# Kernel optimization log

Hardware: AMD Instinct MI355X
Metric: run time of the kernel (lower is better)

The kernel has to match this reference:

```python
import jax, jax.numpy as jnp
import numpy as np
from jax import lax

DIM = 128
N_CODEBOOKS = 8
CODEBOOK_SIZE = 2048
BATCH = 16
TOKENS = 2048


def setup_inputs() -> dict:
    key = jax.random.key(0)
    k1, k2 = jax.random.split(key)
    x = jax.random.normal(k1, (BATCH, DIM, TOKENS), dtype=jnp.float32)
    # matches nn.Parameter(torch.randn(K, D) / D**0.5) per stage, stacked
    codebooks = jax.random.normal(k2, (N_CODEBOOKS, CODEBOOK_SIZE, DIM),
                                  dtype=jnp.float32) / jnp.sqrt(jnp.float32(DIM))
    return {"x": x, "codebooks": codebooks}


def reference(x, codebooks):
    """Residual VQ forward.

    x: (B, D, T), codebooks: (n_cb, K, D)
    Returns (total_quantized (B,D,T), codes (B,n_cb,T) int32, commitment_loss scalar)
    """
    xt = jnp.transpose(x, (0, 2, 1))  # (B, T, D)

    def step(carry, cb):
        residual, total = carry  # (B,T,D) each; cb: (K,D)
        # squared euclidean distances: ||r||^2 - 2 r.c + ||c||^2 -> (B,T,K)
        dist = (jnp.sum(residual * residual, axis=-1, keepdims=True)
                - 2.0 * jnp.einsum('btd,kd->btk', residual, cb)
                + jnp.sum(cb * cb, axis=-1))
        idx = jnp.argmin(dist, axis=-1)          # (B, T)
        quantized = cb[idx]                       # gather -> (B, T, D)
        # straight-through combine
        q_st = residual + lax.stop_gradient(quantized - residual)
        total = total + q_st
        residual = residual - lax.stop_gradient(quantized)
        # F.mse_loss(residual.detach(), zeros) == mean(residual**2), detached
        loss = jnp.mean(lax.stop_gradient(residual) ** 2)
        return (residual, total), (idx.astype(jnp.int32), loss)

    init = (xt, jnp.zeros_like(xt))
    (_, total), (codes, losses) = lax.scan(step, init, codebooks)
    total_quantized = jnp.transpose(total, (0, 2, 1))   # (B, D, T)
    codes = jnp.transpose(codes, (1, 0, 2))             # (B, n_cb, T)
    commitment_loss = jnp.sum(losses)
    return total_quantized, codes, commitment_loss
```

## Files before the change

kernel.cpp:

```cpp
#include <hip/hip_runtime.h>

#define DIM 128
#define NCB 8
#define KSZ 2048
#define BATCH 16
#define TOK 2048
#define NTOK (BATCH * TOK)
#define NELEM (BATCH * DIM * TOK)
#define T_TILE 128
#define NTHR 512
#define CHUNK 32
#define NCHUNK 16
#define GCODES 512

typedef float f32x4 __attribute__((ext_vector_type(4)));
typedef _Float16 f16x8 __attribute__((ext_vector_type(8)));

__global__ void rvq_prep_f16(const float* __restrict__ cbs,
                             _Float16* __restrict__ chf) {
    int i = blockIdx.x * 256 + threadIdx.x;
    chf[i] = (_Float16)cbs[i];
}

__global__ void rvq_cnorm(const float* __restrict__ cbs,
                          float* __restrict__ cnorm,
                          float* __restrict__ loss_acc) {
    if (blockIdx.x == 0 && threadIdx.x == 0) *loss_acc = 0.0f;
    int k = blockIdx.x * 256 + threadIdx.x;
    const float4* row = (const float4*)(cbs + (size_t)k * DIM);
    float s = 0.0f;
#pragma unroll
    for (int i = 0; i < DIM / 4; ++i) {
        float4 v = row[i];
        s += v.x * v.x + v.y * v.y + v.z * v.z + v.w * v.w;
    }
    cnorm[k] = s;
}

__global__ __launch_bounds__(NTHR, 2) void rvq_fused(
        const float* __restrict__ x,
        const float* __restrict__ cbs,
        const _Float16* __restrict__ chf,
        const float* __restrict__ cng,
        float* __restrict__ out,
        float* __restrict__ codes,
        float* __restrict__ loss_acc) {
    __shared__ float res_lds[T_TILE][DIM + 4];
    __shared__ __align__(16) char shbuf[T_TILE * 144 * 4];
    __shared__ float cn_lds[KSZ];

    _Float16* Ball = (_Float16*)shbuf;
    float*    cand = (float*)shbuf;

    const int tid   = threadIdx.x;
    const int lane  = tid & 63;
    const int wv    = __builtin_amdgcn_readfirstlane(tid >> 6);
    const int col16 = lane & 15;
    const int quad  = lane >> 4;
    const int g     = wv >> 1;
    const int sub   = wv & 1;

    const int token0 = blockIdx.x * T_TILE;
    const int b      = token0 >> 11;
    const int t_in_b = token0 & (TOK - 1);

    {
        const float* xb = x + (size_t)b * DIM * TOK + t_in_b;
#pragma unroll
        for (int it = 0; it < 8; ++it) {
            int idx = it * NTHR + tid;
            int d  = idx >> 5;
            int t4 = (idx & 31) * 4;
            float4 v = *(const float4*)(xb + (size_t)d * TOK + t4);
            res_lds[t4 + 0][d] = v.x;
            res_lds[t4 + 1][d] = v.y;
            res_lds[t4 + 2][d] = v.z;
            res_lds[t4 + 3][d] = v.w;
        }
    }
    __syncthreads();

    float my_loss = 0.0f;
    const float INFV = __builtin_inff();

#pragma unroll 1
    for (int s = 0; s < NCB; ++s) {
        const _Float16* __restrict__ ch_s = chf + (size_t)s * KSZ * DIM;
        const float* __restrict__ cb_s = cbs + (size_t)s * KSZ * DIM;
        const float* __restrict__ cn_s = cng + (size_t)s * KSZ;

        {
            float4 v = *(const float4*)(cn_s + tid * 4);
            *(float4*)&cn_lds[tid * 4] = v;
        }

        f16x8 ah[4][4];
#pragma unroll
        for (int mt = 0; mt < 4; ++mt) {
#pragma unroll
            for (int dc = 0; dc < 4; ++dc) {
                int t  = sub * 64 + mt * 16 + col16;
                int d0 = dc * 32 + quad * 8;
                float4 u = *(const float4*)&res_lds[t][d0];
                float4 w = *(const float4*)&res_lds[t][d0 + 4];
                f16x8 hv;
                hv[0] = (_Float16)u.x; hv[1] = (_Float16)u.y;
                hv[2] = (_Float16)u.z; hv[3] = (_Float16)u.w;
                hv[4] = (_Float16)w.x; hv[5] = (_Float16)w.y;
                hv[6] = (_Float16)w.z; hv[7] = (_Float16)w.w;
                ah[mt][dc] = hv;
            }
        }

        float k1[16], k2[16];
#pragma unroll
        for (int sl = 0; sl < 16; ++sl) { k1[sl] = INFV; k2[sl] = INFV; }

        f16x8 stg[4];
        _Float16* Bg = Ball + g * 2 * 4096;

#pragma unroll
        for (int j = 0; j < 4; ++j) {
            int f = sub * 4 + j;
            int nt = f >> 2, dc = f & 3;
            stg[j] = *(const f16x8*)(ch_s +
                (size_t)(g * GCODES + nt * 16 + col16) * DIM + dc * 32 + quad * 8);
        }
#pragma unroll
        for (int j = 0; j < 4; ++j) {
            int f = sub * 4 + j;
            *(f16x8*)(Bg + f * 512 + lane * 8) = stg[j];
        }
        __syncthreads();

        f32x4 acc[4][2];
#pragma unroll 1
        for (int c = 0; c < NCHUNK; ++c) {
            const int cur = c & 1;
            if (c < NCHUNK - 1) {
#pragma unroll
                for (int j = 0; j < 4; ++j) {
                    int f = sub * 4 + j;
                    int nt = f >> 2, dc = f & 3;
                    stg[j] = *(const f16x8*)(ch_s +
                        (size_t)(g * GCODES + (c + 1) * CHUNK + nt * 16 + col16) * DIM
                        + dc * 32 + quad * 8);
                }
            }
#pragma unroll
            for (int mt = 0; mt < 4; ++mt) {
                acc[mt][0] = (f32x4){0.f, 0.f, 0.f, 0.f};
                acc[mt][1] = (f32x4){0.f, 0.f, 0.f, 0.f};
            }
#pragma unroll
            for (int dc = 0; dc < 4; ++dc) {
                f16x8 b0 = *(const f16x8*)(Bg + cur * 4096 + dc * 512 + lane * 8);
                f16x8 b1 = *(const f16x8*)(Bg + cur * 4096 + (4 + dc) * 512 + lane * 8);
#pragma unroll
                for (int mt = 0; mt < 4; ++mt) {
                    acc[mt][0] = __builtin_amdgcn_mfma_f32_16x16x32_f16(
                        ah[mt][dc], b0, acc[mt][0], 0, 0, 0);
                    acc[mt][1] = __builtin_amdgcn_mfma_f32_16x16x32_f16(
                        ah[mt][dc], b1, acc[mt][1], 0, 0, 0);
                }
            }
            {
                float cn0 = cn_lds[g * GCODES + c * CHUNK + col16];
                float cn1 = cn_lds[g * GCODES + c * CHUNK + 16 + col16];
                unsigned em = (unsigned)(c << 1);
#pragma unroll
                for (int mt = 0; mt < 4; ++mt) {
#pragma unroll
                    for (int r = 0; r < 4; ++r) {
                        float p0 = fmaf(-2.0f, acc[mt][0][r], cn0);
                        float p1 = fmaf(-2.0f, acc[mt][1][r], cn1);
                        float q0 = __uint_as_float(
                            (__float_as_uint(p0) & 0xFFFFFFE0u) | em);
                        float q1 = __uint_as_float(
                            (__float_as_uint(p1) & 0xFFFFFFE0u) | em | 1u);
                        float m = fminf(q0, q1);
                        int sl = mt * 4 + r;
                        k2[sl] = fminf(k2[sl], fmaxf(k1[sl], m));
                        k1[sl] = fminf(k1[sl], m);
                    }
                }
            }
            if (c < NCHUNK - 1) {
#pragma unroll
                for (int j = 0; j < 4; ++j) {
                    int f = sub * 4 + j;
                    *(f16x8*)(Bg + (cur ^ 1) * 4096 + f * 512 + lane * 8) = stg[j];
                }
            }
            __syncthreads();
        }

#pragma unroll
        for (int mt = 0; mt < 4; ++mt) {
#pragma unroll
            for (int r = 0; r < 4; ++r) {
                int t = sub * 64 + mt * 16 + quad * 4 + r;
                int sl = mt * 4 + r;
                float2 pr; pr.x = k1[sl]; pr.y = k2[sl];
                *(float2*)&cand[t * 144 + g * 36 + col16 * 2] = pr;
            }
        }
        __syncthreads();

        {
            const int t  = tid >> 2;
            const int gg = tid & 3;
            float bk[4];
            int   bcol[4];
#pragma unroll
            for (int jj = 0; jj < 4; ++jj) { bk[jj] = INFV; bcol[jj] = 0; }
            const float* base = &cand[t * 144 + gg * 36];
#pragma unroll
            for (int j = 0; j < 8; ++j) {
                float4 v4 = *(const float4*)(base + j * 4);
                float vv[4] = {v4.x, v4.y, v4.z, v4.w};
#pragma unroll
                for (int e = 0; e < 4; ++e) {
                    float v = vv[e];
                    int col = (j * 4 + e) >> 1;
#pragma unroll
                    for (int jj = 0; jj < 4; ++jj) {
                        bool lt = v < bk[jj];
                        float tv = bk[jj]; int tc = bcol[jj];
                        bk[jj] = lt ? v : bk[jj];
                        bcol[jj] = lt ? col : bcol[jj];
                        v = lt ? tv : v;
                        col = lt ? tc : col;
                    }
                }
            }
            int cds[4];
#pragma unroll
            for (int jj = 0; jj < 4; ++jj) {
                unsigned e = __float_as_uint(bk[jj]) & 0x1Fu;
                cds[jj] = gg * GCODES + (int)((e >> 1) << 5) +
                          (int)((e & 1) << 4) + bcol[jj];
            }
            const float* p0 = cb_s + (size_t)cds[0] * DIM;
            const float* p1 = cb_s + (size_t)cds[1] * DIM;
            const float* p2 = cb_s + (size_t)cds[2] * DIM;
            const float* p3 = cb_s + (size_t)cds[3] * DIM;
            float n0 = 0, n1 = 0, n2 = 0, n3 = 0;
            float a[4][4];
#pragma unroll
            for (int jj = 0; jj < 4; ++jj)
#pragma unroll
                for (int e = 0; e < 4; ++e) a[jj][e] = 0.0f;
#pragma unroll 8
            for (int d4 = 0; d4 < DIM / 4; ++d4) {
                float4 r4 = *(const float4*)&res_lds[t][d4 * 4];
                n0 = fmaf(r4.x, r4.x, n0); n1 = fmaf(r4.y, r4.y, n1);
                n2 = fmaf(r4.z, r4.z, n2); n3 = fmaf(r4.w, r4.w, n3);
                float4 q0 = *(const float4*)(p0 + d4 * 4);
                a[0][0] = fmaf(r4.x, q0.x, a[0][0]);
                a[0][1] = fmaf(r4.y, q0.y, a[0][1]);
                a[0][2] = fmaf(r4.z, q0.z, a[0][2]);
                a[0][3] = fmaf(r4.w, q0.w, a[0][3]);
                float4 q1 = *(const float4*)(p1 + d4 * 4);
                a[1][0] = fmaf(r4.x, q1.x, a[1][0]);
                a[1][1] = fmaf(r4.y, q1.y, a[1][1]);
                a[1][2] = fmaf(r4.z, q1.z, a[1][2]);
                a[1][3] = fmaf(r4.w, q1.w, a[1][3]);
                float4 q2 = *(const float4*)(p2 + d4 * 4);
                a[2][0] = fmaf(r4.x, q2.x, a[2][0]);
                a[2][1] = fmaf(r4.y, q2.y, a[2][1]);
                a[2][2] = fmaf(r4.z, q2.z, a[2][2]);
                a[2][3] = fmaf(r4.w, q2.w, a[2][3]);
                float4 q3 = *(const float4*)(p3 + d4 * 4);
                a[3][0] = fmaf(r4.x, q3.x, a[3][0]);
                a[3][1] = fmaf(r4.y, q3.y, a[3][1]);
                a[3][2] = fmaf(r4.z, q3.z, a[3][2]);
                a[3][3] = fmaf(r4.w, q3.w, a[3][3]);
            }
            float rn = (n0 + n1) + (n2 + n3);
            float bd = INFV; int bc = 0x7FFFFFFF;
#pragma unroll
            for (int jj = 0; jj < 4; ++jj) {
                float dot = (a[jj][0] + a[jj][1]) + (a[jj][2] + a[jj][3]);
                float dist = fmaf(-2.0f, dot, rn) + cn_s[cds[jj]];
                if (dist < bd || (dist == bd && cds[jj] < bc)) {
                    bd = dist; bc = cds[jj];
                }
            }
#pragma unroll
            for (int mk = 1; mk <= 2; mk <<= 1) {
                float od = __shfl_xor(bd, mk, 64);
                int   oc = __shfl_xor(bc, mk, 64);
                if (od < bd || (od == bd && oc < bc)) { bd = od; bc = oc; }
            }
            if (gg == 0)
                codes[(size_t)b * (NCB * TOK) + (size_t)s * TOK + t_in_b + t] =
                    (float)bc;
            const float* qrow = cb_s + (size_t)bc * DIM;
            float lp = 0.0f;
#pragma unroll
            for (int d4 = 0; d4 < 8; ++d4) {
                int d = gg * 32 + d4 * 4;
                float4 r4 = *(const float4*)&res_lds[t][d];
                float4 q4 = *(const float4*)(qrow + d);
                float4 nr;
                nr.x = r4.x - q4.x; nr.y = r4.y - q4.y;
                nr.z = r4.z - q4.z; nr.w = r4.w - q4.w;
                *(float4*)&res_lds[t][d] = nr;
                lp += nr.x * nr.x + nr.y * nr.y + nr.z * nr.z + nr.w * nr.w;
            }
            my_loss += lp;
        }
        __syncthreads();
    }

    {
        const float* xb = x + (size_t)b * DIM * TOK + t_in_b;
        float* ob = out + (size_t)b * DIM * TOK + t_in_b;
#pragma unroll
        for (int it = 0; it < 8; ++it) {
            int idx = it * NTHR + tid;
            int d  = idx >> 5;
            int t4 = (idx & 31) * 4;
            float4 v = *(const float4*)(xb + (size_t)d * TOK + t4);
            float4 o;
            o.x = v.x - res_lds[t4 + 0][d];
            o.y = v.y - res_lds[t4 + 1][d];
            o.z = v.z - res_lds[t4 + 2][d];
            o.w = v.w - res_lds[t4 + 3][d];
            *(float4*)(ob + (size_t)d * TOK + t4) = o;
        }
    }

#pragma unroll
    for (int off = 32; off > 0; off >>= 1)
        my_loss += __shfl_down(my_loss, off, 64);
    if (lane == 0) atomicAdd(loss_acc, my_loss);
}

__global__ void rvq_loss_fin(const float* __restrict__ loss_acc,
                             float* __restrict__ loss_out) {
    *loss_out = *loss_acc * (1.0f / (float)NELEM);
}

extern "C" void kernel_launch(void* const* d_in, const int* in_sizes, int n_in,
                              void* d_out, int out_size, void* d_ws, size_t ws_size,
                              hipStream_t stream) {
    const float* x   = (const float*)d_in[0];
    const float* cbs = (const float*)d_in[1];

    float* out      = (float*)d_out;
    float* codes    = out + NELEM;
    float* loss_out = out + NELEM + (size_t)BATCH * NCB * TOK;

    float* wsf      = (float*)d_ws;
    float* loss_acc = wsf;
    _Float16* chf   = (_Float16*)(wsf + 256);
    float* cng      = (float*)(chf + (size_t)NCB * KSZ * DIM);

    hipLaunchKernelGGL(rvq_prep_f16, dim3((NCB * KSZ * DIM) / 256), dim3(256),
                       0, stream, cbs, chf);
    hipLaunchKernelGGL(rvq_cnorm, dim3((NCB * KSZ) / 256), dim3(256), 0, stream,
                       cbs, cng, loss_acc);
    hipLaunchKernelGGL(rvq_fused, dim3(NTOK / T_TILE), dim3(NTHR), 0, stream,
                       x, cbs, chf, cng, out, codes, loss_acc);
    hipLaunchKernelGGL(rvq_loss_fin, dim3(1), dim3(1), 0, stream,
                       loss_acc, loss_out);
}
```

Baseline: 603.6 us.

## Load codebook fragments directly from global into registers, drop LDS staging

The f16 codebook fragments now go straight from global memory into MFMA B-operand registers with double-buffered register sets (bA/bB), replacing the LDS staging buffer and the per-chunk __syncthreads. The full 9-bit code index is packed into the low mantissa bits of each distance, so the top-2 tracking and final top-4 selection no longer carry separate column indices and use min/max networks. This removes LDS traffic and barriers from the inner loop, and the candidate buffer shrinks. The cost is more global/L2 loads, because the two waves in each pair now each load the full fragment set, plus higher register pressure and coarser distance precision from truncating 9 mantissa bits.

Measured after the change: 606.3 us. About the same (+0.4%).

```diff
diff --git a/kernel.cpp b/kernel.cpp
--- a/kernel.cpp
+++ b/kernel.cpp
@@ -46,11 +46,8 @@
         float* __restrict__ codes,
         float* __restrict__ loss_acc) {
     __shared__ float res_lds[T_TILE][DIM + 4];
-    __shared__ __align__(16) char shbuf[T_TILE * 144 * 4];
+    __shared__ float cand[T_TILE * 132];
     __shared__ float cn_lds[KSZ];
-
-    _Float16* Ball = (_Float16*)shbuf;
-    float*    cand = (float*)shbuf;
 
     const int tid   = threadIdx.x;
     const int lane  = tid & 63;
@@ -83,16 +80,71 @@
     float my_loss = 0.0f;
     const float INFV = __builtin_inff();
 
+#define LOADB(dst)                                                             \
+    {                                                                          \
+        _Pragma("unroll")                                                      \
+        for (int dc = 0; dc < 4; ++dc) {                                       \
+            dst[dc]     = *(const f16x8*)(p0 + dc * 32);                       \
+            dst[4 + dc] = *(const f16x8*)(p1 + dc * 32);                       \
+        }                                                                      \
+    }
+
+#define COMPUTE(bX)                                                            \
+    {                                                                          \
+        _Pragma("unroll")                                                      \
+        for (int mt = 0; mt < 4; ++mt) {                                       \
+            acc[mt][0] = (f32x4){0.f, 0.f, 0.f, 0.f};                          \
+            acc[mt][1] = (f32x4){0.f, 0.f, 0.f, 0.f};                          \
+        }                                                                      \
+        _Pragma("unroll")                                                      \
+        for (int dc = 0; dc < 4; ++dc) {                                       \
+            _Pragma("unroll")                                                  \
+            for (int mt = 0; mt < 4; ++mt) {                                   \
+                acc[mt][0] = __builtin_amdgcn_mfma_f32_16x16x32_f16(           \
+                    ah[mt][dc], bX[dc], acc[mt][0], 0, 0, 0);                  \
+                acc[mt][1] = __builtin_amdgcn_mfma_f32_16x16x32_f16(           \
+                    ah[mt][dc], bX[4 + dc], acc[mt][1], 0, 0, 0);              \
+            }                                                                  \
+        }                                                                      \
+    }
+
+#define FOLD(cc)                                                               \
+    {                                                                          \
+        float cn0 = cn_lds[g * GCODES + (cc) * CHUNK + col16];                 \
+        float cn1 = cn_lds[g * GCODES + (cc) * CHUNK + 16 + col16];            \
+        unsigned em0 = ((unsigned)(cc) << 5) | (unsigned)col16;                \
+        unsigned em1 = em0 | 16u;                                              \
+        _Pragma("unroll")                                                      \
+        for (int mt = 0; mt < 4; ++mt) {                                       \
+            _Pragma("unroll")                                                  \
+            for (int r = 0; r < 4; ++r) {                                      \
+                int sl = mt * 4 + r;                                           \
+                float p0s = fmaf(-2.0f, acc[mt][0][r], cn0);                   \
+                float p1s = fmaf(-2.0f, acc[mt][1][r], cn1);                   \
+                float q0 = __uint_as_float(                                    \
+                    (__float_as_uint(p0s) & 0xFFFFFE00u) | em0);               \
+                float q1 = __uint_as_float(                                    \
+                    (__float_as_uint(p1s) & 0xFFFFFE00u) | em1);               \
+                k2[sl] = fminf(k2[sl], fmaxf(k1[sl], q0));                     \
+                k1[sl] = fminf(k1[sl], q0);                                    \
+                k2[sl] = fminf(k2[sl], fmaxf(k1[sl], q1));                     \
+                k1[sl] = fminf(k1[sl], q1);                                    \
+            }                                                                  \
+        }                                                                      \
+    }
+
 #pragma unroll 1
     for (int s = 0; s < NCB; ++s) {
         const _Float16* __restrict__ ch_s = chf + (size_t)s * KSZ * DIM;
         const float* __restrict__ cb_s = cbs + (size_t)s * KSZ * DIM;
         const float* __restrict__ cn_s = cng + (size_t)s * KSZ;
 
-        {
-            float4 v = *(const float4*)(cn_s + tid * 4);
-            *(float4*)&cn_lds[tid * 4] = v;
-        }
+        const _Float16* p0 = ch_s + (size_t)(g * GCODES + col16) * DIM + quad * 8;
+        const _Float16* p1 = p0 + 16 * DIM;
+        f16x8 bA[8], bB[8];
+        LOADB(bA);
+
+        *(float4*)&cn_lds[tid * 4] = *(const float4*)(cn_s + tid * 4);
 
         f16x8 ah[4][4];
 #pragma unroll
@@ -116,83 +168,21 @@
 #pragma unroll
         for (int sl = 0; sl < 16; ++sl) { k1[sl] = INFV; k2[sl] = INFV; }
 
-        f16x8 stg[4];
-        _Float16* Bg = Ball + g * 2 * 4096;
-
-#pragma unroll
-        for (int j = 0; j < 4; ++j) {
-            int f = sub * 4 + j;
-            int nt = f >> 2, dc = f & 3;
-            stg[j] = *(const f16x8*)(ch_s +
-                (size_t)(g * GCODES + nt * 16 + col16) * DIM + dc * 32 + quad * 8);
-        }
-#pragma unroll
-        for (int j = 0; j < 4; ++j) {
-            int f = sub * 4 + j;
-            *(f16x8*)(Bg + f * 512 + lane * 8) = stg[j];
-        }
         __syncthreads();
 
         f32x4 acc[4][2];
 #pragma unroll 1
-        for (int c = 0; c < NCHUNK; ++c) {
-            const int cur = c & 1;
-            if (c < NCHUNK - 1) {
-#pragma unroll
-                for (int j = 0; j < 4; ++j) {
-                    int f = sub * 4 + j;
-                    int nt = f >> 2, dc = f & 3;
-                    stg[j] = *(const f16x8*)(ch_s +
-                        (size_t)(g * GCODES + (c + 1) * CHUNK + nt * 16 + col16) * DIM
-                        + dc * 32 + quad * 8);
-                }
-            }
-#pragma unroll
-            for (int mt = 0; mt < 4; ++mt) {
-                acc[mt][0] = (f32x4){0.f, 0.f, 0.f, 0.f};
-                acc[mt][1] = (f32x4){0.f, 0.f, 0.f, 0.f};
-            }
-#pragma unroll
-            for (int dc = 0; dc < 4; ++dc) {
-                f16x8 b0 = *(const f16x8*)(Bg + cur * 4096 + dc * 512 + lane * 8);
-                f16x8 b1 = *(const f16x8*)(Bg + cur * 4096 + (4 + dc) * 512 + lane * 8);
-#pragma unroll
-                for (int mt = 0; mt < 4; ++mt) {
-                    acc[mt][0] = __builtin_amdgcn_mfma_f32_16x16x32_f16(
-                        ah[mt][dc], b0, acc[mt][0], 0, 0, 0);
-                    acc[mt][1] = __builtin_amdgcn_mfma_f32_16x16x32_f16(
-                        ah[mt][dc], b1, acc[mt][1], 0, 0, 0);
-                }
-            }
-            {
-                float cn0 = cn_lds[g * GCODES + c * CHUNK + col16];
-                float cn1 = cn_lds[g * GCODES + c * CHUNK + 16 + col16];
-                unsigned em = (unsigned)(c << 1);
-#pragma unroll
-                for (int mt = 0; mt < 4; ++mt) {
-#pragma unroll
-                    for (int r = 0; r < 4; ++r) {
-                        float p0 = fmaf(-2.0f, acc[mt][0][r], cn0);
-                        float p1 = fmaf(-2.0f, acc[mt][1][r], cn1);
-                        float q0 = __uint_as_float(
-                            (__float_as_uint(p0) & 0xFFFFFFE0u) | em);
-                        float q1 = __uint_as_float(
-                            (__float_as_uint(p1) & 0xFFFFFFE0u) | em | 1u);
-                        float m = fminf(q0, q1);
-                        int sl = mt * 4 + r;
-                        k2[sl] = fminf(k2[sl], fmaxf(k1[sl], m));
-                        k1[sl] = fminf(k1[sl], m);
-                    }
-                }
-            }
-            if (c < NCHUNK - 1) {
-#pragma unroll
-                for (int j = 0; j < 4; ++j) {
-                    int f = sub * 4 + j;
-                    *(f16x8*)(Bg + (cur ^ 1) * 4096 + f * 512 + lane * 8) = stg[j];
-                }
-            }
-            __syncthreads();
+        for (int c = 0; c < NCHUNK; c += 2) {
+            p0 += CHUNK * DIM; p1 += CHUNK * DIM;
+            LOADB(bB);
+            COMPUTE(bA);
+            FOLD(c);
+            if (c + 2 < NCHUNK) {
+                p0 += CHUNK * DIM; p1 += CHUNK * DIM;
+                LOADB(bA);
+            }
+            COMPUTE(bB);
+            FOLD(c + 1);
         }
 
 #pragma unroll
@@ -202,7 +192,7 @@
                 int t = sub * 64 + mt * 16 + quad * 4 + r;
                 int sl = mt * 4 + r;
                 float2 pr; pr.x = k1[sl]; pr.y = k2[sl];
-                *(float2*)&cand[t * 144 + g * 36 + col16 * 2] = pr;
+                *(float2*)&cand[t * 132 + g * 32 + col16 * 2] = pr;
             }
         }
         __syncthreads();
@@ -210,11 +200,8 @@
         {
             const int t  = tid >> 2;
             const int gg = tid & 3;
-            float bk[4];
-            int   bcol[4];
-#pragma unroll
-            for (int jj = 0; jj < 4; ++jj) { bk[jj] = INFV; bcol[jj] = 0; }
-            const float* base = &cand[t * 144 + gg * 36];
+            float bk0 = INFV, bk1 = INFV, bk2 = INFV, bk3 = INFV;
+            const float* base = &cand[t * 132 + gg * 32];
 #pragma unroll
             for (int j = 0; j < 8; ++j) {
                 float4 v4 = *(const float4*)(base + j * 4);
@@ -222,29 +209,22 @@
 #pragma unroll
                 for (int e = 0; e < 4; ++e) {
                     float v = vv[e];
-                    int col = (j * 4 + e) >> 1;
-#pragma unroll
-                    for (int jj = 0; jj < 4; ++jj) {
-                        bool lt = v < bk[jj];
-                        float tv = bk[jj]; int tc = bcol[jj];
-                        bk[jj] = lt ? v : bk[jj];
-                        bcol[jj] = lt ? col : bcol[jj];
-                        v = lt ? tv : v;
-                        col = lt ? tc : col;
-                    }
+                    float M0 = fmaxf(bk0, v);  bk0 = fminf(bk0, v);
+                    float M1 = fmaxf(bk1, M0); bk1 = fminf(bk1, M0);
+                    float M2 = fmaxf(bk2, M1); bk2 = fminf(bk2, M1);
+                    bk3 = fminf(bk3, M2);
                 }
             }
             int cds[4];
-#pragma unroll
-            for (int jj = 0; jj < 4; ++jj) {
-                unsigned e = __float_as_uint(bk[jj]) & 0x1Fu;
-                cds[jj] = gg * GCODES + (int)((e >> 1) << 5) +
-                          (int)((e & 1) << 4) + bcol[jj];
-            }
-            const float* p0 = cb_s + (size_t)cds[0] * DIM;
-            const float* p1 = cb_s + (size_t)cds[1] * DIM;
-            const float* p2 = cb_s + (size_t)cds[2] * DIM;
-            const float* p3 = cb_s + (size_t)cds[3] * DIM;
+            cds[0] = gg * GCODES + (int)(__float_as_uint(bk0) & 0x1FFu);
+            cds[1] = gg * GCODES + (int)(__float_as_uint(bk1) & 0x1FFu);
+            cds[2] = gg * GCODES + (int)(__float_as_uint(bk2) & 0x1FFu);
+            cds[3] = gg * GCODES + (int)(__float_as_uint(bk3) & 0x1FFu);
+
+            const float* q1p = cb_s + (size_t)cds[0] * DIM;
+            const float* q2p = cb_s + (size_t)cds[1] * DIM;
+            const float* q3p = cb_s + (size_t)cds[2] * DIM;
+            const float* q4p = cb_s + (size_t)cds[3] * DIM;
             float n0 = 0, n1 = 0, n2 = 0, n3 = 0;
             float a[4][4];
 #pragma unroll
@@ -256,22 +236,22 @@
                 float4 r4 = *(const float4*)&res_lds[t][d4 * 4];
                 n0 = fmaf(r4.x, r4.x, n0); n1 = fmaf(r4.y, r4.y, n1);
                 n2 = fmaf(r4.z, r4.z, n2); n3 = fmaf(r4.w, r4.w, n3);
-                float4 q0 = *(const float4*)(p0 + d4 * 4);
+                float4 q0 = *(const float4*)(q1p + d4 * 4);
                 a[0][0] = fmaf(r4.x, q0.x, a[0][0]);
                 a[0][1] = fmaf(r4.y, q0.y, a[0][1]);
                 a[0][2] = fmaf(r4.z, q0.z, a[0][2]);
                 a[0][3] = fmaf(r4.w, q0.w, a[0][3]);
-                float4 q1 = *(const float4*)(p1 + d4 * 4);
+                float4 q1 = *(const float4*)(q2p + d4 * 4);
                 a[1][0] = fmaf(r4.x, q1.x, a[1][0]);
                 a[1][1] = fmaf(r4.y, q1.y, a[1][1]);
                 a[1][2] = fmaf(r4.z, q1.z, a[1][2]);
                 a[1][3] = fmaf(r4.w, q1.w, a[1][3]);
-                float4 q2 = *(const float4*)(p2 + d4 * 4);
+                float4 q2 = *(const float4*)(q3p + d4 * 4);
                 a[2][0] = fmaf(r4.x, q2.x, a[2][0]);
                 a[2][1] = fmaf(r4.y, q2.y, a[2][1]);
                 a[2][2] = fmaf(r4.z, q2.z, a[2][2]);
                 a[2][3] = fmaf(r4.w, q2.w, a[2][3]);
-                float4 q3 = *(const float4*)(p3 + d4 * 4);
+                float4 q3 = *(const float4*)(q4p + d4 * 4);
                 a[3][0] = fmaf(r4.x, q3.x, a[3][0]);
                 a[3][1] = fmaf(r4.y, q3.y, a[3][1]);
                 a[3][2] = fmaf(r4.z, q3.z, a[3][2]);
```
